# Performance work log

Hardware: AMD Instinct MI355X
Metric: run time of the kernel (lower is better)

Reference implementation:

```python
import jax, jax.numpy as jnp
import numpy as np

N_NODES = 50000
N_EDGES = 1600000
D_IN = 48
D_OUT = 48


def setup_inputs() -> dict:
    key = jax.random.key(0)
    k1, k2, k3, k4 = jax.random.split(key, 4)
    features = jax.random.normal(k1, (N_NODES, D_IN), dtype=jnp.float32)
    src = jax.random.randint(k2, (N_EDGES,), 0, N_NODES, dtype=jnp.int64)
    dst = jax.random.randint(k3, (N_EDGES,), 0, N_NODES, dtype=jnp.int64)
    # xavier_normal for Linear(48,48): std = sqrt(2/(fan_in+fan_out))
    std = np.sqrt(2.0 / (D_IN + D_OUT))
    W = jax.random.normal(k4, (D_OUT, D_IN), dtype=jnp.float32) * std
    b = jnp.zeros((D_OUT,), dtype=jnp.float32)
    return {"features": features, "src": src, "dst": dst, "W": W, "b": b}


def reference(features, src, dst, W, b):
    n = features.shape[0]
    ones = jnp.ones(src.shape[0], dtype=features.dtype)
    out_deg = jax.ops.segment_sum(ones, src, num_segments=n)
    in_deg = jax.ops.segment_sum(ones, dst, num_segments=n)
    ci = jax.lax.rsqrt(jnp.maximum(out_deg, 1.0))  # per src node
    cj = jax.lax.rsqrt(jnp.maximum(in_deg, 1.0))   # per dst node
    # gather-scale: m_e = h[src_e] * ci[src_e]
    msg = features[src] * ci[src][:, None]          # [E, D_IN]
    # scatter-sum to dst, then scale by cj
    agg = jax.ops.segment_sum(msg, dst, num_segments=n) * cj[:, None]
    # DGL update_all leaves zero-in-degree nodes with their original 'h'
    h = jnp.where(in_deg[:, None] > 0, agg, features)
    out = jax.nn.relu(h @ W.T + b)
    return out
```

## Files before the change

### kernel.cpp

```cpp
#include <hip/hip_runtime.h>
#include <hip/hip_fp16.h>

#define N_NODES 50000
#define N_EDGES 1600000
#define D 48

#define EPB 8192
#define PB  196
#define NPB_D 50
#define NBIN_D 1000
#define NPB_S 256
#define NBIN_S 196

#define EMAX 2400
#define HS 52

#define RECD_OFF  0
#define SRCB_OFF  6422528
#define OFFLD_OFF 8028160
#define OFFLS_OFF 8420552
#define CI_OFF    8497776
#define SFEAT_OFF 8697776
#define SFEAT_END 13497776

__global__ __launch_bounds__(1024) void k_prep(const int* __restrict__ src,
                                               const int* __restrict__ dst,
                                               unsigned int* __restrict__ rec,
                                               unsigned char* __restrict__ srcb,
                                               unsigned short* __restrict__ offld,
                                               unsigned short* __restrict__ offls) {
    __shared__ int cd[NBIN_D];
    __shared__ int cs[NBIN_S];
    __shared__ int wsum[16], wexcl[16];
    __shared__ int wsum2[4], wexcl2[4];
    __shared__ alignas(16) unsigned int  bufd[EPB];
    __shared__ alignas(16) unsigned char bufs[EPB];
    int tid = threadIdx.x, p = blockIdx.x;
    int wave = tid >> 6, lane = tid & 63;
    int base = p * EPB;

    int sv[8], dv[8];
    bool ok[8];
    const int4* s4p = (const int4*)src;
    const int4* d4p = (const int4*)dst;
    #pragma unroll
    for (int c = 0; c < 2; ++c) {
        int e4 = base + c * 4096 + tid * 4;
        bool v = (e4 < N_EDGES);
        int4 s4 = v ? s4p[e4 >> 2] : make_int4(0, 0, 0, 0);
        int4 d4 = v ? d4p[e4 >> 2] : make_int4(0, 0, 0, 0);
        sv[c * 4 + 0] = s4.x; sv[c * 4 + 1] = s4.y;
        sv[c * 4 + 2] = s4.z; sv[c * 4 + 3] = s4.w;
        dv[c * 4 + 0] = d4.x; dv[c * 4 + 1] = d4.y;
        dv[c * 4 + 2] = d4.z; dv[c * 4 + 3] = d4.w;
        ok[c * 4 + 0] = v; ok[c * 4 + 1] = v; ok[c * 4 + 2] = v; ok[c * 4 + 3] = v;
    }

    for (int i = tid; i < NBIN_D; i += 1024) cd[i] = 0;
    for (int i = tid; i < NBIN_S; i += 1024) cs[i] = 0;
    __syncthreads();
    #pragma unroll
    for (int k = 0; k < 8; ++k) {
        if (ok[k]) {
            atomicAdd(&cd[dv[k] / NPB_D], 1);
            atomicAdd(&cs[sv[k] >> 8], 1);
        }
    }
    __syncthreads();

    int own = (tid < NBIN_D) ? cd[tid] : 0;
    int incl = own;
    #pragma unroll
    for (int o = 1; o < 64; o <<= 1) {
        int u = __shfl_up(incl, o);
        if (lane >= o) incl += u;
    }
    if (lane == 63) wsum[wave] = incl;
    __syncthreads();
    if (tid < 16) {
        int v = wsum[tid];
        int ic = v;
        #pragma unroll
        for (int o = 1; o < 16; o <<= 1) {
            int u = __shfl_up(ic, o);
            if (lane >= o) ic += u;
        }
        wexcl[tid] = ic - v;
    }
    __syncthreads();
    if (tid < NBIN_D) {
        int gincl = wexcl[wave] + incl;
        int ex = gincl - own;
        offld[p * (NBIN_D + 1) + tid] = (unsigned short)ex;
        cd[tid] = ex;
        if (tid == NBIN_D - 1) offld[p * (NBIN_D + 1) + NBIN_D] = (unsigned short)gincl;
    }

    int own2 = (tid < NBIN_S) ? cs[tid] : 0;
    int incl2 = own2;
    #pragma unroll
    for (int o = 1; o < 64; o <<= 1) {
        int u = __shfl_up(incl2, o);
        if (lane >= o) incl2 += u;
    }
    if (lane == 63 && wave < 4) wsum2[wave] = incl2;
    __syncthreads();
    if (tid < 4) {
        int v = wsum2[tid];
        int ic = v;
        #pragma unroll
        for (int o = 1; o < 4; o <<= 1) {
            int u = __shfl_up(ic, o);
            if (lane >= o) ic += u;
        }
        wexcl2[tid] = ic - v;
    }
    __syncthreads();
    if (tid < NBIN_S) {
        int gincl2 = wexcl2[wave] + incl2;
        int ex = gincl2 - own2;
        offls[p * (NBIN_S + 1) + tid] = (unsigned short)ex;
        cs[tid] = ex;
        if (tid == NBIN_S - 1) offls[p * (NBIN_S + 1) + NBIN_S] = (unsigned short)gincl2;
    }
    __syncthreads();

    #pragma unroll
    for (int k = 0; k < 8; ++k) {
        if (ok[k]) {
            int s = sv[k], d = dv[k];
            int bin = d / NPB_D;
            int pd = atomicAdd(&cd[bin], 1);
            bufd[pd] = ((unsigned int)s << 6) | (unsigned int)(d - bin * NPB_D);
            int ps = atomicAdd(&cs[s >> 8], 1);
            bufs[ps] = (unsigned char)s;
        }
    }
    __syncthreads();

    int4* ro = (int4*)(rec + base);
    const int4* bi = (const int4*)bufd;
    for (int i = tid; i < EPB / 4; i += 1024) ro[i] = bi[i];
    unsigned int* so = (unsigned int*)(srcb + base);
    const unsigned int* bs = (const unsigned int*)bufs;
    for (int i = tid; i < EPB / 4; i += 1024) so[i] = bs[i];
}

__global__ __launch_bounds__(512) void k_ci(const unsigned char* __restrict__ srcb,
                                            const unsigned short* __restrict__ offls,
                                            const float* __restrict__ feat,
                                            float* __restrict__ ci,
                                            __half* __restrict__ sfeat,
                                            int do_scale) {
    __shared__ int cnt[NPB_S];
    __shared__ float cl[NPB_S];
    int tid = threadIdx.x, sb = blockIdx.x;
    for (int i = tid; i < NPB_S; i += 512) cnt[i] = 0;
    __syncthreads();
    int wave = tid >> 6, lane = tid & 63;
    for (int p = wave; p < PB; p += 8) {
        int beg = offls[p * (NBIN_S + 1) + sb];
        int end = offls[p * (NBIN_S + 1) + sb + 1];
        for (int j = beg + lane; j < end; j += 64)
            atomicAdd(&cnt[srcb[p * EPB + j]], 1);
    }
    __syncthreads();
    if (tid < NPB_S) {
        float c = rsqrtf(fmaxf((float)cnt[tid], 1.0f));
        cl[tid] = c;
        int n = sb * NPB_S + tid;
        if (n < N_NODES) ci[n] = c;
    }
    __syncthreads();
    if (do_scale) {
        int nb = sb * NPB_S;
        int lim2 = (min(NPB_S, N_NODES - nb)) * 24;
        const float2* f2 = (const float2*)feat + (size_t)nb * 24;
        __half2* s2 = (__half2*)sfeat + (size_t)nb * 24;
        for (int i = tid; i < lim2; i += 512) {
            float sc = cl[i / 24];
            float2 f = f2[i];
            s2[i] = __float22half2_rn(make_float2(f.x * sc, f.y * sc));
        }
    }
}

template <bool PRESCALED>
__global__ __launch_bounds__(512, 8) void k_gcn(
    const unsigned int* __restrict__ rec, const unsigned short* __restrict__ offld,
    const float* __restrict__ ci, const __half* __restrict__ sfeat,
    const float* __restrict__ feat,
    const float* __restrict__ W, const float* __restrict__ b,
    float* __restrict__ out) {
    __shared__ int   colb[EMAX];
    __shared__ float hl[NPB_D * HS];
    __shared__ float Wl[D * HS];
    __shared__ float bl[D];
    __shared__ int   ideg[NPB_D];
    __shared__ int   off[NPB_D];
    __shared__ int   cur[NPB_D];
    __shared__ int   runoff[PB + 1];
    __shared__ int   runpos[PB];
    __shared__ int   wsum[8], wexcl[8];
    int tid = threadIdx.x, bin = blockIdx.x;
    int wave = tid >> 6, lane = tid & 63;

    for (int i = tid; i < D * D; i += 512) Wl[(i / D) * HS + (i % D)] = W[i];
    if (tid < D) bl[tid] = b[tid];
    if (tid < NPB_D) { ideg[tid] = 0; cur[tid] = 0; }

    int rlen = 0;
    if (tid < PB) {
        int o0 = offld[tid * (NBIN_D + 1) + bin];
        int o1 = offld[tid * (NBIN_D + 1) + bin + 1];
        rlen = o1 - o0;
        runpos[tid] = tid * EPB + o0;
    }
    int incl = rlen;
    #pragma unroll
    for (int o = 1; o < 64; o <<= 1) {
        int u = __shfl_up(incl, o);
        if (lane >= o) incl += u;
    }
    if (lane == 63) wsum[wave] = incl;
    __syncthreads();
    if (tid < 8) {
        int v = wsum[tid];
        int ic = v;
        #pragma unroll
        for (int o = 1; o < 8; o <<= 1) {
            int u = __shfl_up(ic, o);
            if (lane >= o) ic += u;
        }
        wexcl[tid] = ic - v;
        if (tid == 7) runoff[PB] = ic;
    }
    __syncthreads();
    if (tid < PB) runoff[tid] = wexcl[wave] + incl - rlen;
    __syncthreads();
    int cnt = runoff[PB];
    if (cnt > EMAX) cnt = EMAX;

    unsigned int rr[5];
    #pragma unroll
    for (int k = 0; k < 5; ++k) {
        int j = tid + k * 512;
        rr[k] = 0xFFFFFFFFu;
        if (j < cnt) {
            int lo = 0, hi = PB - 1;
            while (lo < hi) {
                int mid = (lo + hi + 1) >> 1;
                if (runoff[mid] <= j) lo = mid; else hi = mid - 1;
            }
            unsigned int r = rec[runpos[lo] + (j - runoff[lo])];
            rr[k] = r;
            atomicAdd(&ideg[r & 63], 1);
        }
    }
    __syncthreads();
    if (tid < NPB_D) {
        int v = ideg[tid];
        int ic = v;
        #pragma unroll
        for (int o = 1; o < 64; o <<= 1) {
            int u = __shfl_up(ic, o);
            if (tid >= o) ic += u;
        }
        off[tid] = ic - v;
    }
    __syncthreads();
    #pragma unroll
    for (int k = 0; k < 5; ++k) {
        if (rr[k] != 0xFFFFFFFFu) {
            int dl = rr[k] & 63;
            int p = atomicAdd(&cur[dl], 1);
            colb[off[dl] + p] = (int)(rr[k] >> 6);
        }
    }
    __syncthreads();

    int eslot = lane >> 3;
    int d8 = lane & 7;
    bool lane_ok = (d8 < 6);
    const float4* feat4 = (const float4*)feat;
    const uint4* sf = (const uint4*)sfeat;

    for (int q = 0; q < 7; ++q) {
        int nl = q * 8 + wave;
        if (nl >= NPB_D) break;
        int n = bin * NPB_D + nl;
        int cb = off[nl];
        int deg = ideg[nl];

        float4 accA = make_float4(0.0f, 0.0f, 0.0f, 0.0f);
        float4 accB = make_float4(0.0f, 0.0f, 0.0f, 0.0f);
        for (int i0 = 0; i0 < deg; i0 += 8) {
            int ei = i0 + eslot;
            bool act = lane_ok && (ei < deg);
            int s = act ? colb[cb + ei] : 0;
            if (act) {
                if (PRESCALED) {
                    uint4 u = sf[(size_t)s * 6 + d8];
                    __half2 h0 = *reinterpret_cast<__half2*>(&u.x);
                    __half2 h1 = *reinterpret_cast<__half2*>(&u.y);
                    __half2 h2 = *reinterpret_cast<__half2*>(&u.z);
                    __half2 h3 = *reinterpret_cast<__half2*>(&u.w);
                    float2 f0 = __half22float2(h0);
                    float2 f1 = __half22float2(h1);
                    float2 f2 = __half22float2(h2);
                    float2 f3 = __half22float2(h3);
                    accA.x += f0.x; accA.y += f0.y; accA.z += f1.x; accA.w += f1.y;
                    accB.x += f2.x; accB.y += f2.y; accB.z += f3.x; accB.w += f3.y;
                } else {
                    float c = ci[s];
                    float4 fa = feat4[(size_t)s * 12 + d8 * 2];
                    float4 fb = feat4[(size_t)s * 12 + d8 * 2 + 1];
                    accA.x = fmaf(fa.x, c, accA.x);
                    accA.y = fmaf(fa.y, c, accA.y);
                    accA.z = fmaf(fa.z, c, accA.z);
                    accA.w = fmaf(fa.w, c, accA.w);
                    accB.x = fmaf(fb.x, c, accB.x);
                    accB.y = fmaf(fb.y, c, accB.y);
                    accB.z = fmaf(fb.z, c, accB.z);
                    accB.w = fmaf(fb.w, c, accB.w);
                }
            }
        }
        #pragma unroll
        for (int m = 8; m <= 32; m <<= 1) {
            accA.x += __shfl_xor(accA.x, m);
            accA.y += __shfl_xor(accA.y, m);
            accA.z += __shfl_xor(accA.z, m);
            accA.w += __shfl_xor(accA.w, m);
            accB.x += __shfl_xor(accB.x, m);
            accB.y += __shfl_xor(accB.y, m);
            accB.z += __shfl_xor(accB.z, m);
            accB.w += __shfl_xor(accB.w, m);
        }
        if (lane < 6) {
            float4 rA, rB;
            if (deg > 0) {
                float cj = rsqrtf((float)deg);
                rA = make_float4(accA.x * cj, accA.y * cj, accA.z * cj, accA.w * cj);
                rB = make_float4(accB.x * cj, accB.y * cj, accB.z * cj, accB.w * cj);
            } else {
                rA = feat4[(size_t)n * 12 + lane * 2];
                rB = feat4[(size_t)n * 12 + lane * 2 + 1];
            }
            *(float4*)(hl + nl * HS + lane * 8) = rA;
            *(float4*)(hl + nl * HS + lane * 8 + 4) = rB;
        }
    }
    __syncthreads();

    #pragma unroll
    for (int half = 0; half < 2; ++half) {
        int nl = (tid >> 4) + half * 32;
        int c = tid & 15;
        if (nl < NPB_D) {
            int n = bin * NPB_D + nl;
            float a0 = bl[c], a1 = bl[c + 16], a2 = bl[c + 32];
            #pragma unroll
            for (int k4 = 0; k4 < 12; ++k4) {
                float4 hv = *(const float4*)(hl + nl * HS + k4 * 4);
                float4 w0 = *(const float4*)(Wl + c * HS + k4 * 4);
                float4 w1 = *(const float4*)(Wl + (c + 16) * HS + k4 * 4);
                float4 w2 = *(const float4*)(Wl + (c + 32) * HS + k4 * 4);
                a0 = fmaf(hv.x, w0.x, a0); a0 = fmaf(hv.y, w0.y, a0);
                a0 = fmaf(hv.z, w0.z, a0); a0 = fmaf(hv.w, w0.w, a0);
                a1 = fmaf(hv.x, w1.x, a1); a1 = fmaf(hv.y, w1.y, a1);
                a1 = fmaf(hv.z, w1.z, a1); a1 = fmaf(hv.w, w1.w, a1);
                a2 = fmaf(hv.x, w2.x, a2); a2 = fmaf(hv.y, w2.y, a2);
                a2 = fmaf(hv.z, w2.z, a2); a2 = fmaf(hv.w, w2.w, a2);
            }
            float* op = out + (size_t)n * D;
            op[c]      = fmaxf(a0, 0.0f);
            op[c + 16] = fmaxf(a1, 0.0f);
            op[c + 32] = fmaxf(a2, 0.0f);
        }
    }
}

extern "C" void kernel_launch(void* const* d_in, const int* in_sizes, int n_in,
                              void* d_out, int out_size, void* d_ws, size_t ws_size,
                              hipStream_t stream) {
    const float* feat = (const float*)d_in[0];
    const int*   src  = (const int*)d_in[1];
    const int*   dst  = (const int*)d_in[2];
    const float* W    = (const float*)d_in[3];
    const float* b    = (const float*)d_in[4];
    float* out = (float*)d_out;

    char* ws = (char*)d_ws;
    unsigned int*   rec   = (unsigned int*)(ws + RECD_OFF);
    unsigned char*  srcb  = (unsigned char*)(ws + SRCB_OFF);
    unsigned short* offld = (unsigned short*)(ws + OFFLD_OFF);
    unsigned short* offls = (unsigned short*)(ws + OFFLS_OFF);
    float*          ci    = (float*)(ws + CI_OFF);
    __half*         sfeat = (__half*)(ws + SFEAT_OFF);

    const bool prescale = (ws_size >= (size_t)SFEAT_END);

    k_prep<<<PB, 1024, 0, stream>>>(src, dst, rec, srcb, offld, offls);
    k_ci<<<NBIN_S, 512, 0, stream>>>(srcb, offls, feat, ci, sfeat, prescale ? 1 : 0);
    if (prescale)
        k_gcn<true><<<NBIN_D, 512, 0, stream>>>(rec, offld, ci, sfeat, feat, W, b, out);
    else
        k_gcn<false><<<NBIN_D, 512, 0, stream>>>(rec, offld, ci, sfeat, feat, W, b, out);
}
```

Baseline: 140.5 us.

## Compute out-degree with global atomics instead of source-binning pass

Replaces the second counting-sort of edges by source bin (the shared-memory histogram, scan, scatter and srcb buffer) with direct global atomicAdd into a per-node out-degree array cleared by a memset. The ci/prescale kernel becomes a flat elementwise kernel that reads the degree and scales features with float4 loads. This removes the srcb writes and re-reads and the extra scan in k_prep. In exchange it adds 1.6M contended global atomics and an extra memset launch.

```diff
diff --git a/kernel.cpp b/kernel.cpp
--- a/kernel.cpp
+++ b/kernel.cpp
@@ -9,32 +9,25 @@
 #define PB  196
 #define NPB_D 50
 #define NBIN_D 1000
-#define NPB_S 256
-#define NBIN_S 196
 
 #define EMAX 2400
 #define HS 52
 
 #define RECD_OFF  0
-#define SRCB_OFF  6422528
-#define OFFLD_OFF 8028160
-#define OFFLS_OFF 8420552
-#define CI_OFF    8497776
-#define SFEAT_OFF 8697776
-#define SFEAT_END 13497776
+#define OFFLD_OFF 6422528
+#define ODEG_OFF  6815232
+#define CI_OFF    7015424
+#define SFEAT_OFF 7215616
+#define SFEAT_END 12015616
 
 __global__ __launch_bounds__(1024) void k_prep(const int* __restrict__ src,
                                                const int* __restrict__ dst,
                                                unsigned int* __restrict__ rec,
-                                               unsigned char* __restrict__ srcb,
                                                unsigned short* __restrict__ offld,
-                                               unsigned short* __restrict__ offls) {
+                                               int* __restrict__ odeg) {
     __shared__ int cd[NBIN_D];
-    __shared__ int cs[NBIN_S];
     __shared__ int wsum[16], wexcl[16];
-    __shared__ int wsum2[4], wexcl2[4];
-    __shared__ alignas(16) unsigned int  bufd[EPB];
-    __shared__ alignas(16) unsigned char bufs[EPB];
+    __shared__ alignas(16) unsigned int bufd[EPB];
     int tid = threadIdx.x, p = blockIdx.x;
     int wave = tid >> 6, lane = tid & 63;
     int base = p * EPB;
@@ -57,13 +50,12 @@
     }
 
     for (int i = tid; i < NBIN_D; i += 1024) cd[i] = 0;
-    for (int i = tid; i < NBIN_S; i += 1024) cs[i] = 0;
     __syncthreads();
     #pragma unroll
     for (int k = 0; k < 8; ++k) {
         if (ok[k]) {
             atomicAdd(&cd[dv[k] / NPB_D], 1);
-            atomicAdd(&cs[sv[k] >> 8], 1);
+            atomicAdd(&odeg[sv[k]], 1);
         }
     }
     __syncthreads();
@@ -95,34 +87,6 @@
         cd[tid] = ex;
         if (tid == NBIN_D - 1) offld[p * (NBIN_D + 1) + NBIN_D] = (unsigned short)gincl;
     }
-
-    int own2 = (tid < NBIN_S) ? cs[tid] : 0;
-    int incl2 = own2;
-    #pragma unroll
-    for (int o = 1; o < 64; o <<= 1) {
-        int u = __shfl_up(incl2, o);
-        if (lane >= o) incl2 += u;
-    }
-    if (lane == 63 && wave < 4) wsum2[wave] = incl2;
-    __syncthreads();
-    if (tid < 4) {
-        int v = wsum2[tid];
-        int ic = v;
-        #pragma unroll
-        for (int o = 1; o < 4; o <<= 1) {
-            int u = __shfl_up(ic, o);
-            if (lane >= o) ic += u;
-        }
-        wexcl2[tid] = ic - v;
-    }
-    __syncthreads();
-    if (tid < NBIN_S) {
-        int gincl2 = wexcl2[wave] + incl2;
-        int ex = gincl2 - own2;
-        offls[p * (NBIN_S + 1) + tid] = (unsigned short)ex;
-        cs[tid] = ex;
-        if (tid == NBIN_S - 1) offls[p * (NBIN_S + 1) + NBIN_S] = (unsigned short)gincl2;
-    }
     __syncthreads();
 
     #pragma unroll
@@ -132,8 +96,6 @@
             int bin = d / NPB_D;
             int pd = atomicAdd(&cd[bin], 1);
             bufd[pd] = ((unsigned int)s << 6) | (unsigned int)(d - bin * NPB_D);
-            int ps = atomicAdd(&cs[s >> 8], 1);
-            bufs[ps] = (unsigned char)s;
         }
     }
     __syncthreads();
@@ -141,47 +103,26 @@
     int4* ro = (int4*)(rec + base);
     const int4* bi = (const int4*)bufd;
     for (int i = tid; i < EPB / 4; i += 1024) ro[i] = bi[i];
-    unsigned int* so = (unsigned int*)(srcb + base);
-    const unsigned int* bs = (const unsigned int*)bufs;
-    for (int i = tid; i < EPB / 4; i += 1024) so[i] = bs[i];
 }
 
-__global__ __launch_bounds__(512) void k_ci(const unsigned char* __restrict__ srcb,
-                                            const unsigned short* __restrict__ offls,
+__global__ __launch_bounds__(512) void k_ci(const int* __restrict__ odeg,
                                             const float* __restrict__ feat,
                                             float* __restrict__ ci,
                                             __half* __restrict__ sfeat,
                                             int do_scale) {
-    __shared__ int cnt[NPB_S];
-    __shared__ float cl[NPB_S];
-    int tid = threadIdx.x, sb = blockIdx.x;
-    for (int i = tid; i < NPB_S; i += 512) cnt[i] = 0;
-    __syncthreads();
-    int wave = tid >> 6, lane = tid & 63;
-    for (int p = wave; p < PB; p += 8) {
-        int beg = offls[p * (NBIN_S + 1) + sb];
-        int end = offls[p * (NBIN_S + 1) + sb + 1];
-        for (int j = beg + lane; j < end; j += 64)
-            atomicAdd(&cnt[srcb[p * EPB + j]], 1);
-    }
-    __syncthreads();
-    if (tid < NPB_S) {
-        float c = rsqrtf(fmaxf((float)cnt[tid], 1.0f));
-        cl[tid] = c;
-        int n = sb * NPB_S + tid;
-        if (n < N_NODES) ci[n] = c;
-    }
-    __syncthreads();
+    int i = blockIdx.x * 512 + threadIdx.x;
+    if (i >= N_NODES * 12) return;
+    int n = i / 12;
+    float sc = rsqrtf(fmaxf((float)odeg[n], 1.0f));
+    if (i - n * 12 == 0) ci[n] = sc;
     if (do_scale) {
-        int nb = sb * NPB_S;
-        int lim2 = (min(NPB_S, N_NODES - nb)) * 24;
-        const float2* f2 = (const float2*)feat + (size_t)nb * 24;
-        __half2* s2 = (__half2*)sfeat + (size_t)nb * 24;
-        for (int i = tid; i < lim2; i += 512) {
-            float sc = cl[i / 24];
-            float2 f = f2[i];
-            s2[i] = __float22half2_rn(make_float2(f.x * sc, f.y * sc));
-        }
+        float4 f = ((const float4*)feat)[i];
+        __half2 h0 = __float22half2_rn(make_float2(f.x * sc, f.y * sc));
+        __half2 h1 = __float22half2_rn(make_float2(f.z * sc, f.w * sc));
+        uint2 u;
+        u.x = *(unsigned int*)&h0;
+        u.y = *(unsigned int*)&h1;
+        ((uint2*)sfeat)[i] = u;
     }
 }
 
@@ -393,16 +334,17 @@
 
     char* ws = (char*)d_ws;
     unsigned int*   rec   = (unsigned int*)(ws + RECD_OFF);
-    unsigned char*  srcb  = (unsigned char*)(ws + SRCB_OFF);
     unsigned short* offld = (unsigned short*)(ws + OFFLD_OFF);
-    unsigned short* offls = (unsigned short*)(ws + OFFLS_OFF);
+    int*            odeg  = (int*)(ws + ODEG_OFF);
     float*          ci    = (float*)(ws + CI_OFF);
     __half*         sfeat = (__half*)(ws + SFEAT_OFF);
 
     const bool prescale = (ws_size >= (size_t)SFEAT_END);
 
-    k_prep<<<PB, 1024, 0, stream>>>(src, dst, rec, srcb, offld, offls);
-    k_ci<<<NBIN_S, 512, 0, stream>>>(srcb, offls, feat, ci, sfeat, prescale ? 1 : 0);
+    hipMemsetAsync(odeg, 0, (size_t)N_NODES * sizeof(int), stream);
+    k_prep<<<PB, 1024, 0, stream>>>(src, dst, rec, offld, odeg);
+    k_ci<<<(N_NODES * 12 + 511) / 512, 512, 0, stream>>>(odeg, feat, ci, sfeat,
+                                                         prescale ? 1 : 0);
     if (prescale)
         k_gcn<true><<<NBIN_D, 512, 0, stream>>>(rec, offld, ci, sfeat, feat, W, b, out);
     else
```

New measurement: 188.1 us. 1.34x slower.
